# Kernel tuning notes

Measured on AMD Instinct MI355X. Metric: run time of the kernel, lower is better.

The kernel has to match this reference:

```python
import jax, jax.numpy as jnp
import numpy as np

B, N, DIM, HEADS, GAMMA = 16384, 4, 512, 8, 0.4
SCALE = DIM ** -0.5

def _mask_and_bias():
    pos = np.array([[0, 0], [0, 1], [1, 0], [1, 1]], dtype=np.float32)
    dist = np.linalg.norm(pos[:, None] - pos[None, :], axis=-1)  # [4,4]
    M = (dist <= 1.0).astype(np.float32)
    # P[i, j] = -(j+1)*gamma where dist[i,j] > 1, else 0
    P = np.where(dist > 1.0, -(np.arange(1, 5, dtype=np.float32)[None, :]) * GAMMA, 0.0).astype(np.float32)
    return jnp.asarray(M), jnp.asarray(P)

M_MASK, P_BIAS = _mask_and_bias()

def setup_inputs() -> dict:
    key = jax.random.key(0)
    ks = jax.random.split(key, 8)
    s = 0.02
    return {
        "x": jax.random.normal(ks[0], (B, N, DIM), jnp.float32),
        "context": jax.random.normal(ks[1], (B, N, DIM), jnp.float32),
        "Wq": jax.random.normal(ks[2], (DIM, DIM), jnp.float32) * s,
        "bq": jax.random.normal(ks[3], (DIM,), jnp.float32) * s,
        "Wkv": jax.random.normal(ks[4], (DIM, 2 * DIM), jnp.float32) * s,
        "bkv": jax.random.normal(ks[5], (2 * DIM,), jnp.float32) * s,
        "Wo": jax.random.normal(ks[6], (DIM, DIM), jnp.float32) * s,
        "bo": jax.random.normal(ks[7], (DIM,), jnp.float32) * s,
    }

def reference(x, context, Wq, bq, Wkv, bkv, Wo, bo):
    b, n, d = x.shape
    h = HEADS
    dh = d // h
    q = x @ Wq + bq                      # [b, n, d]
    kv = context @ Wkv + bkv             # [b, n, 2d]
    k, v = jnp.split(kv, 2, axis=-1)
    # b n (h dh) -> b h n dh
    q = q.reshape(b, n, h, dh).transpose(0, 2, 1, 3)
    k = k.reshape(b, n, h, dh).transpose(0, 2, 1, 3)
    v = v.reshape(b, n, h, dh).transpose(0, 2, 1, 3)
    attn = jnp.einsum('bhid,bhjd->bhij', q, k) * SCALE
    attn = attn * M_MASK + P_BIAS        # mask then additive positional bias
    attn = jax.nn.softmax(attn, axis=-1)
    attn = attn * M_MASK                 # post-softmax mask
    out = jnp.einsum('bhij,bhjd->bhid', attn, v)
    out = out.transpose(0, 2, 1, 3).reshape(b, n, d)
    return out @ Wo + bo
```

## Files before the change

kernel.cpp:

```cpp
#include <hip/hip_runtime.h>
#include <cstdint>
#include <cstddef>


typedef __attribute__((ext_vector_type(8))) short short8;
typedef __attribute__((ext_vector_type(4))) float floatx4;

__device__ __forceinline__ unsigned short f2bf(float f) {
    unsigned u = __float_as_uint(f);
    unsigned r = 0x7fffu + ((u >> 16) & 1u);
    return (unsigned short)((u + r) >> 16);
}
__device__ __forceinline__ float bf2f(unsigned short h) {
    return __uint_as_float(((unsigned)h) << 16);
}

__device__ __forceinline__ void async_cp16(const unsigned short* g, unsigned short* l) {
    __builtin_amdgcn_global_load_lds(
        (const __attribute__((address_space(1))) unsigned int*)g,
        (__attribute__((address_space(3))) unsigned int*)l, 16, 0, 0);
}

__global__ void transpose_cast_kernel(const float* __restrict__ in,
                                      unsigned short* __restrict__ out,
                                      int K, int N) {
    __shared__ float tile[32][33];
    const int kb = blockIdx.x * 32, nb = blockIdx.y * 32;
    const int t = threadIdx.x, c = t & 31, r = t >> 5;
#pragma unroll
    for (int i = 0; i < 4; ++i) {
        int kl = r + 8 * i;
        tile[kl][c] = in[(size_t)(kb + kl) * N + nb + c];
    }
    __syncthreads();
#pragma unroll
    for (int i = 0; i < 4; ++i) {
        int nl = r + 8 * i;
        out[(size_t)(nb + nl) * K + kb + c] = f2bf(tile[c][nl]);
    }
}

__global__ void cast_bf16_kernel(const float* __restrict__ in,
                                 unsigned short* __restrict__ out) {
    const int i = (int)blockIdx.x * 256 + threadIdx.x;
    float4 a = ((const float4*)in)[2 * i];
    float4 b = ((const float4*)in)[2 * i + 1];
    short8 p;
    p[0] = (short)f2bf(a.x); p[1] = (short)f2bf(a.y);
    p[2] = (short)f2bf(a.z); p[3] = (short)f2bf(a.w);
    p[4] = (short)f2bf(b.x); p[5] = (short)f2bf(b.y);
    p[6] = (short)f2bf(b.z); p[7] = (short)f2bf(b.w);
    ((short8*)out)[i] = p;
}

template <bool OUT_F32>
__global__ __launch_bounds__(256, 2)
void gemm_kernel(const unsigned short* __restrict__ A, int lda,
                 const unsigned short* __restrict__ Wt,
                 const float* __restrict__ bias,
                 void* __restrict__ Cv, int ldc,
                 int K, int xshift) {
    constexpr int BK = 64;
    __shared__ __align__(16) unsigned short As[128 * 64];
    __shared__ __align__(16) unsigned short Bs[128 * 64];
    const int t = threadIdx.x;
    const int wave = t >> 6, lane = t & 63;
    const int lm = lane & 15, quad = lane >> 4;

    const int NXB = 1 << xshift;
    const int lin = (int)blockIdx.x + ((int)blockIdx.y << xshift);
    const int xcd = lin & 7, slot = lin >> 3;
    const int by = xcd * 64 + (slot >> xshift);
    const int bx = slot & (NXB - 1);
    const int row0 = by * 128, n0 = bx * 128;
    const int wm = (wave & 1) * 64, wn = (wave >> 1) * 64;

    const int arow = t >> 3;
    const int cb = (t & 7) ^ (arow & 7);
    const unsigned short* Ag = A + (size_t)(row0 + arow) * lda + cb * 8;
    const unsigned short* Bg = Wt + (size_t)(n0 + arow) * K + cb * 8;

    floatx4 acc[4][4] = {};

    for (int kb = 0; kb < K; kb += BK) {
        __syncthreads();
#pragma unroll
        for (int it = 0; it < 4; ++it) {
            async_cp16(Ag + kb + (size_t)(it * 32) * lda,
                       &As[(it * 256 + wave * 64) * 8]);
            async_cp16(Bg + kb + (size_t)(it * 32) * K,
                       &Bs[(it * 256 + wave * 64) * 8]);
        }
        __syncthreads();
#pragma unroll
        for (int kk = 0; kk < 2; ++kk) {
            short8 af[4], bfv[4];
            const int cfrag = kk * 4 + quad;
            const int csw = cfrag ^ (lm & 7);
#pragma unroll
            for (int mi = 0; mi < 4; ++mi)
                af[mi] = *(const short8*)&As[(wm + mi * 16 + lm) * 64 + csw * 8];
#pragma unroll
            for (int ni = 0; ni < 4; ++ni)
                bfv[ni] = *(const short8*)&Bs[(wn + ni * 16 + lm) * 64 + csw * 8];
#pragma unroll
            for (int mi = 0; mi < 4; ++mi)
#pragma unroll
                for (int ni = 0; ni < 4; ++ni)
                    acc[mi][ni] = __builtin_amdgcn_mfma_f32_16x16x32_bf16(
                        af[mi], bfv[ni], acc[mi][ni], 0, 0, 0);
        }
    }
#pragma unroll
    for (int ni = 0; ni < 4; ++ni) {
        int col = n0 + wn + ni * 16 + lm;
        float bv = bias[col];
#pragma unroll
        for (int mi = 0; mi < 4; ++mi) {
            int rowb = row0 + wm + mi * 16 + quad * 4;
#pragma unroll
            for (int r = 0; r < 4; ++r) {
                float v = acc[mi][ni][r] + bv;
                if (OUT_F32)
                    ((float*)Cv)[(size_t)(rowb + r) * ldc + col] = v;
                else
                    ((unsigned short*)Cv)[(size_t)(rowb + r) * ldc + col] = f2bf(v);
            }
        }
    }
}

__global__ __launch_bounds__(256)
void attn_kernel(unsigned short* __restrict__ qkv) {
    const int t = threadIdx.x;
    const int wave = t >> 6, lane = t & 63;
    const int bh = (int)blockIdx.x * 4 + wave;
    const int b = bh >> 3, h = bh & 7;
    const float scale = 0.044194173824159216f;
    const size_t base = (size_t)b * 4 * 1536 + h * 64 + lane;
    float qv[4], kk4[4], vv[4];
#pragma unroll
    for (int i = 0; i < 4; ++i) {
        qv[i]  = bf2f(qkv[base + (size_t)i * 1536]);
        kk4[i] = bf2f(qkv[base + (size_t)i * 1536 + 512]);
        vv[i]  = bf2f(qkv[base + (size_t)i * 1536 + 1024]);
    }
    float s[4][4];
#pragma unroll
    for (int i = 0; i < 4; ++i)
#pragma unroll
        for (int j = 0; j < 4; ++j) {
            float v = qv[i] * kk4[j];
#pragma unroll
            for (int off = 32; off > 0; off >>= 1) v += __shfl_xor(v, off, 64);
            s[i][j] = v * scale;
        }
    const float Mm[4][4] = {{1,1,1,0},{1,1,0,1},{1,0,1,1},{0,1,1,1}};
    const float Pp[4][4] = {{0,0,0,-1.6f},{0,0,-1.2f,0},{0,-0.8f,0,0},{-0.4f,0,0,0}};
#pragma unroll
    for (int i = 0; i < 4; ++i) {
        float tj[4], mx = -1e30f;
#pragma unroll
        for (int j = 0; j < 4; ++j) {
            tj[j] = s[i][j] * Mm[i][j] + Pp[i][j];
            mx = fmaxf(mx, tj[j]);
        }
        float e[4], sum = 0.f;
#pragma unroll
        for (int j = 0; j < 4; ++j) { e[j] = __expf(tj[j] - mx); sum += e[j]; }
        float inv = 1.f / sum;
        float od = 0.f;
#pragma unroll
        for (int j = 0; j < 4; ++j) od += e[j] * Mm[i][j] * vv[j];
        qkv[base + (size_t)i * 1536] = f2bf(od * inv);
    }
}

extern "C" void kernel_launch(void* const* d_in, const int* in_sizes, int n_in,
                              void* d_out, int out_size, void* d_ws, size_t ws_size,
                              hipStream_t stream) {
    const float* x   = (const float*)d_in[0];
    const float* ctx = (const float*)d_in[1];
    const float* Wq  = (const float*)d_in[2];
    const float* bq  = (const float*)d_in[3];
    const float* Wkv = (const float*)d_in[4];
    const float* bkv = (const float*)d_in[5];
    const float* Wo  = (const float*)d_in[6];
    const float* bo  = (const float*)d_in[7];
    float* out = (float*)d_out;

    const int M = 65536;
    unsigned short* WqkvT = (unsigned short*)d_ws;
    unsigned short* WoT   = WqkvT + 1536 * 512;
    unsigned short* abf   = WoT + 512 * 512;
    unsigned short* qkv   = abf + (size_t)M * 512;

    dim3 b256(256);
    transpose_cast_kernel<<<dim3(16, 16), b256, 0, stream>>>(Wq, WqkvT, 512, 512);
    transpose_cast_kernel<<<dim3(16, 32), b256, 0, stream>>>(Wkv, WqkvT + 512 * 512, 512, 1024);
    transpose_cast_kernel<<<dim3(16, 16), b256, 0, stream>>>(Wo, WoT, 512, 512);

    cast_bf16_kernel<<<dim3(M * 512 / (8 * 256)), b256, 0, stream>>>(x, abf);
    gemm_kernel<false><<<dim3(4, 512), b256, 0, stream>>>(
        abf, 512, WqkvT, bq, qkv, 1536, 512, 2);

    cast_bf16_kernel<<<dim3(M * 512 / (8 * 256)), b256, 0, stream>>>(ctx, abf);
    gemm_kernel<false><<<dim3(8, 512), b256, 0, stream>>>(
        abf, 512, WqkvT + 512 * 512, bkv, qkv + 512, 1536, 512, 3);

    attn_kernel<<<dim3(M * 8 / 16), b256, 0, stream>>>(qkv);

    gemm_kernel<true><<<dim3(4, 512), b256, 0, stream>>>(
        qkv, 1536, WoT, bo, out, 512, 512, 2);
}
```

Baseline: 627.8 us.

## Restructure attention kernel to one wave per batch with vectorized 16-byte loads

The attention kernel now assigns one wave per batch element instead of per (batch, head). Each lane loads 8 contiguous bf16 values as a short8, so every head spans 8 lanes. Dot products become per-lane partial sums over 8 elements followed by a 3-step shuffle reduction, replacing the 6-step full-wave reduction and the 2-byte scalar loads and stores. This is meant to cut shuffle count and memory transactions in the attention stage, at the cost of more registers per lane.

```diff
diff --git a/kernel.cpp b/kernel.cpp
--- a/kernel.cpp
+++ b/kernel.cpp
@@ -134,29 +134,44 @@
 void attn_kernel(unsigned short* __restrict__ qkv) {
     const int t = threadIdx.x;
     const int wave = t >> 6, lane = t & 63;
-    const int bh = (int)blockIdx.x * 4 + wave;
-    const int b = bh >> 3, h = bh & 7;
+    const int b = (int)blockIdx.x * 4 + wave;
     const float scale = 0.044194173824159216f;
-    const size_t base = (size_t)b * 4 * 1536 + h * 64 + lane;
-    float qv[4], kk4[4], vv[4];
-#pragma unroll
-    for (int i = 0; i < 4; ++i) {
-        qv[i]  = bf2f(qkv[base + (size_t)i * 1536]);
-        kk4[i] = bf2f(qkv[base + (size_t)i * 1536 + 512]);
-        vv[i]  = bf2f(qkv[base + (size_t)i * 1536 + 1024]);
-    }
+    const size_t rowbase = (size_t)b * 4 * 1536 + lane * 8;
+
+    short8 qv[4], kv8[4], vv[4];
+#pragma unroll
+    for (int i = 0; i < 4; ++i) {
+        const size_t r = rowbase + (size_t)i * 1536;
+        qv[i]  = *(const short8*)&qkv[r];
+        kv8[i] = *(const short8*)&qkv[r + 512];
+        vv[i]  = *(const short8*)&qkv[r + 1024];
+    }
+    float qf[4][8], kf[4][8];
+#pragma unroll
+    for (int i = 0; i < 4; ++i)
+#pragma unroll
+        for (int e = 0; e < 8; ++e) {
+            qf[i][e] = bf2f((unsigned short)qv[i][e]);
+            kf[i][e] = bf2f((unsigned short)kv8[i][e]);
+        }
+
     float s[4][4];
 #pragma unroll
     for (int i = 0; i < 4; ++i)
 #pragma unroll
         for (int j = 0; j < 4; ++j) {
-            float v = qv[i] * kk4[j];
-#pragma unroll
-            for (int off = 32; off > 0; off >>= 1) v += __shfl_xor(v, off, 64);
-            s[i][j] = v * scale;
-        }
+            float p = 0.f;
+#pragma unroll
+            for (int e = 0; e < 8; ++e) p += qf[i][e] * kf[j][e];
+            p += __shfl_xor(p, 1, 64);
+            p += __shfl_xor(p, 2, 64);
+            p += __shfl_xor(p, 4, 64);
+            s[i][j] = p * scale;
+        }
+
     const float Mm[4][4] = {{1,1,1,0},{1,1,0,1},{1,0,1,1},{0,1,1,1}};
     const float Pp[4][4] = {{0,0,0,-1.6f},{0,0,-1.2f,0},{0,-0.8f,0,0},{-0.4f,0,0,0}};
+    float w[4][4];
 #pragma unroll
     for (int i = 0; i < 4; ++i) {
         float tj[4], mx = -1e30f;
@@ -169,10 +184,24 @@
 #pragma unroll
         for (int j = 0; j < 4; ++j) { e[j] = __expf(tj[j] - mx); sum += e[j]; }
         float inv = 1.f / sum;
-        float od = 0.f;
-#pragma unroll
-        for (int j = 0; j < 4; ++j) od += e[j] * Mm[i][j] * vv[j];
-        qkv[base + (size_t)i * 1536] = f2bf(od * inv);
+#pragma unroll
+        for (int j = 0; j < 4; ++j) w[i][j] = e[j] * Mm[i][j] * inv;
+    }
+
+#pragma unroll
+    for (int i = 0; i < 4; ++i) {
+        float o[8] = {};
+#pragma unroll
+        for (int j = 0; j < 4; ++j) {
+            const float wj = w[i][j];
+#pragma unroll
+            for (int e = 0; e < 8; ++e)
+                o[e] += wj * bf2f((unsigned short)vv[j][e]);
+        }
+        short8 ov;
+#pragma unroll
+        for (int e = 0; e < 8; ++e) ov[e] = (short)f2bf(o[e]);
+        *(short8*)&qkv[rowbase + (size_t)i * 1536] = ov;
     }
 }
 
@@ -208,7 +237,7 @@
     gemm_kernel<false><<<dim3(8, 512), b256, 0, stream>>>(
         abf, 512, WqkvT + 512 * 512, bkv, qkv + 512, 1536, 512, 3);
 
-    attn_kernel<<<dim3(M * 8 / 16), b256, 0, stream>>>(qkv);
+    attn_kernel<<<dim3(16384 / 4), b256, 0, stream>>>(qkv);
 
     gemm_kernel<true><<<dim3(4, 512), b256, 0, stream>>>(
         qkv, 1536, WoT, bo, out, 512, 512, 2);
```

After: 545.1 us. -13.2%, faster.
